# Kernel tuning notes

Measured on AMD Instinct MI355X. Metric: run time of the kernel, lower is better.

Reference implementation:

```python
import jax, jax.numpy as jnp
import numpy as np

B, S, D, V = 64, 16, 2048, 128000


def setup_inputs() -> dict:
    key = jax.random.key(0)
    k1, k2, k3, k4, k5 = jax.random.split(key, 5)
    embedding = jax.random.normal(k1, (V, D), dtype=jnp.float32) * 0.02
    hidden_states = jax.random.normal(k2, (B, S, D), dtype=jnp.float32)
    output_positions = jnp.array([S - 1], dtype=jnp.int32)  # sample from last position
    temperatures = jax.random.uniform(k3, (B,), dtype=jnp.float32, minval=0.5, maxval=1.5)
    top_ps = jax.random.uniform(k4, (B,), dtype=jnp.float32, minval=0.7, maxval=1.0)
    top_ks = jax.random.randint(k5, (B,), 1, 64).astype(jnp.int32)
    return {
        "embedding": embedding,
        "hidden_states": hidden_states,
        "output_positions": output_positions,
        "temperatures": temperatures,
        "top_ps": top_ps,
        "top_ks": top_ks,
    }


def reference(embedding, hidden_states, output_positions, temperatures, top_ps, top_ks):
    # select output position: [B, S, D] -> [B, D]
    hs = jnp.take(hidden_states, output_positions, axis=1)[:, 0, :]
    # vocab logits: [B, V]
    logits = jnp.einsum("bd,vd->bv", hs, embedding)
    logits = logits / temperatures[:, None]
    probs = jax.nn.softmax(logits.astype(jnp.float32), axis=-1)
    # descending sort of probs
    order = jnp.argsort(-probs, axis=-1)                       # [B, V]
    probs_sort = jnp.take_along_axis(probs, order, axis=-1)    # [B, V] descending
    cum = jnp.cumsum(probs_sort, axis=-1)
    # top-p: zero everything whose exclusive-prefix mass exceeds top_p
    probs_sort = jnp.where((cum - probs_sort) > top_ps[:, None], 0.0, probs_sort)
    # top-k: keep only first top_k sorted entries
    ranks = jnp.arange(V, dtype=jnp.int32)[None, :]
    probs_sort = jnp.where(ranks >= top_ks[:, None], 0.0, probs_sort)
    # renormalize
    probs_sort = probs_sort / jnp.sum(probs_sort, axis=-1, keepdims=True)
    # scatter back to original vocab order via inverse permutation
    inv = jnp.argsort(order, axis=-1)
    probs_final = jnp.take_along_axis(probs_sort, inv, axis=-1)
    # multinomial sampling (one token per row); zeros -> log 0 = -inf, excluded
    skey = jax.random.key(42)
    next_token_ids = jax.random.categorical(skey, jnp.log(probs_final), axis=-1)
    return next_token_ids
```

## Files before the change

kernel.cpp:

```cpp
#include <hip/hip_runtime.h>
#include <math.h>

#define BATCH 64
#define SEQ 16
#define DIM 2048
#define VOCAB 128000

#define BM 64
#define BN 128
#define BK 32
#define NT (DIM / BK)

typedef __attribute__((ext_vector_type(8))) short bf16x8;
typedef __attribute__((ext_vector_type(4))) float f32x4;

__device__ __forceinline__ unsigned cvt_pk_bf16(float a, float b) {
  unsigned r;
  asm("v_cvt_pk_bf16_f32 %0, %1, %2" : "=v"(r) : "v"(a), "v"(b));
  return r;
}

__device__ __forceinline__ void split8(float4 x0, float4 x1, bf16x8* hi, bf16x8* lo) {
  float f[8] = {x0.x, x0.y, x0.z, x0.w, x1.x, x1.y, x1.z, x1.w};
  union { unsigned u[4]; bf16x8 v; } H, L;
#pragma unroll
  for (int w = 0; w < 4; ++w) {
    float a = f[2 * w], b = f[2 * w + 1];
    unsigned hp = cvt_pk_bf16(a, b);
    float ha = __uint_as_float(hp << 16);
    float hb = __uint_as_float(hp & 0xffff0000u);
    H.u[w] = hp;
    L.u[w] = cvt_pk_bf16(a - ha, b - hb);
  }
  *hi = H.v;
  *lo = L.v;
}

__device__ __forceinline__ void gload_lds16(const float* src, float* lds_dst) {
  __builtin_amdgcn_global_load_lds(
      (const __attribute__((address_space(1))) void*)src,
      (__attribute__((address_space(3))) void*)lds_dst, 16, 0, 0);
}

__global__ __launch_bounds__(256, 3) void logits_kernel(
    const float* __restrict__ emb,
    const float* __restrict__ hs,
    const int* __restrict__ pos,
    const float* __restrict__ temps,
    float* __restrict__ logits) {
  __shared__ float ldsA[BM * BK];
  __shared__ float ldsB[BN * BK];

  const int tid = threadIdx.x;
  const int lane = tid & 63;
  const int wid = tid >> 6;
  const int lrow = lane & 15;
  const int lkb = lane >> 4;
  const int vb = blockIdx.x * BN + wid * 32;
  const int p = pos[0];

  const int r8 = (lane >> 3) & 7;
  const int c8 = lane & 7;
  const int cswz = 4 * (c8 ^ r8);

  const float* aSrc[2];
  float* aDst[2];
#pragma unroll
  for (int q = 0; q < 2; ++q) {
    const int g = wid * 2 + q;
    const int R = g * 8 + r8;
    aSrc[q] = hs + ((size_t)R * SEQ + p) * DIM + cswz;
    aDst[q] = &ldsA[g * 8 * BK];
  }
  const float* bSrc[4];
  float* bDst[4];
#pragma unroll
  for (int q = 0; q < 4; ++q) {
    const int g = wid * 4 + q;
    const int R = g * 8 + r8;
    bSrc[q] = emb + (size_t)(blockIdx.x * BN + R) * DIM + cswz;
    bDst[q] = &ldsB[g * 8 * BK];
  }

  f32x4 acc[4][2];
#pragma unroll
  for (int i = 0; i < 4; ++i)
#pragma unroll
    for (int j = 0; j < 2; ++j) acc[i][j] = (f32x4){0.f, 0.f, 0.f, 0.f};

  const int sfr = 4 * (lrow & 7);
  const int off0 = (lkb * 8) ^ sfr;
  const int off1 = off0 ^ 4;

  for (int t = 0; t < NT; ++t) {
    const int kof = t * BK;
#pragma unroll
    for (int q = 0; q < 2; ++q) gload_lds16(aSrc[q] + kof, aDst[q]);
#pragma unroll
    for (int q = 0; q < 4; ++q) gload_lds16(bSrc[q] + kof, bDst[q]);
    __syncthreads();

    bf16x8 ah[4], al[4], bh[2], bl[2];
#pragma unroll
    for (int i = 0; i < 4; ++i) {
      const float* rb = &ldsA[(16 * i + lrow) * BK];
      split8(*(const float4*)(rb + off0), *(const float4*)(rb + off1),
             &ah[i], &al[i]);
    }
#pragma unroll
    for (int j = 0; j < 2; ++j) {
      const float* rb = &ldsB[(wid * 32 + 16 * j + lrow) * BK];
      split8(*(const float4*)(rb + off0), *(const float4*)(rb + off1),
             &bh[j], &bl[j]);
    }
#pragma unroll
    for (int i = 0; i < 4; ++i)
#pragma unroll
      for (int j = 0; j < 2; ++j) {
        acc[i][j] = __builtin_amdgcn_mfma_f32_16x16x32_bf16(ah[i], bh[j], acc[i][j], 0, 0, 0);
        acc[i][j] = __builtin_amdgcn_mfma_f32_16x16x32_bf16(ah[i], bl[j], acc[i][j], 0, 0, 0);
        acc[i][j] = __builtin_amdgcn_mfma_f32_16x16x32_bf16(al[i], bh[j], acc[i][j], 0, 0, 0);
      }
    __syncthreads();
  }

#pragma unroll
  for (int i = 0; i < 4; ++i)
#pragma unroll
    for (int r = 0; r < 4; ++r) {
      const int b = 16 * i + lkb * 4 + r;
      const float tt = temps[b];
#pragma unroll
      for (int j = 0; j < 2; ++j) {
        const int v = vb + 16 * j + lrow;
        logits[(size_t)b * VOCAB + v] = acc[i][j][r] / tt;
      }
    }
}

__device__ __forceinline__ void threefry2x32(unsigned k0, unsigned k1,
                                             unsigned x0, unsigned x1,
                                             unsigned* o0, unsigned* o1) {
  const unsigned k2 = k0 ^ k1 ^ 0x1BD11BDAu;
  const unsigned ks[3] = {k0, k1, k2};
  const int rotA[4] = {13, 15, 26, 6};
  const int rotB[4] = {17, 29, 16, 24};
  x0 += k0;
  x1 += k1;
#pragma unroll
  for (int i = 0; i < 5; ++i) {
    const int* rr = (i & 1) ? rotB : rotA;
#pragma unroll
    for (int q = 0; q < 4; ++q) {
      x0 += x1;
      x1 = (x1 << rr[q]) | (x1 >> (32 - rr[q]));
      x1 ^= x0;
    }
    x0 += ks[(i + 1) % 3];
    x1 += ks[(i + 2) % 3] + (unsigned)(i + 1);
  }
  *o0 = x0;
  *o1 = x1;
}

__device__ float gumbel_noise(unsigned flat) {
  unsigned o0, o1;
  threefry2x32(0u, 42u, 0u, flat, &o0, &o1);
  unsigned bits = o0 ^ o1;
  unsigned fb = (bits >> 9) | 0x3f800000u;
  float u = __uint_as_float(fb) - 1.0f;
  const float tiny = 1.17549435e-38f;
  u = fmaxf(u, tiny);
  return -logf(-logf(u));
}

#define CAP 4096
#define NL 12
#define NTH 1024
#define NWAVE 16

__device__ __forceinline__ unsigned sortkey(float x) {
  unsigned bits = __float_as_uint(x);
  return (bits & 0x80000000u) ? ~bits : (bits | 0x80000000u);
}
__device__ __forceinline__ float inv_sortkey(unsigned u) {
  unsigned bits = (u & 0x80000000u) ? (u & 0x7fffffffu) : ~u;
  return __uint_as_float(bits);
}

__global__ __launch_bounds__(NTH) void sample_kernel(
    const float* __restrict__ logits,
    const float* __restrict__ top_ps,
    const int* __restrict__ top_ks,
    const float* __restrict__ temps,
    const int* __restrict__ pos,
    int ws_ok,
    int* __restrict__ out) {
  const int b = blockIdx.x;
  const int tid = threadIdx.x;
  const int lane = tid & 63;
  const int wave = tid >> 6;
  const float* row = logits + (size_t)b * VOCAB;
  const float4* row4 = (const float4*)row;
  const int N4 = VOCAB / 4;

  __shared__ float sred[NWAVE];
  __shared__ int scnt_sh[NL];
  __shared__ float smax, sz;
  __shared__ float sdelta;
  __shared__ unsigned scnt;
  __shared__ unsigned ubuf[CAP];
  __shared__ unsigned ibuf[CAP];
  __shared__ unsigned sorted_u[64];
  __shared__ unsigned sorted_i[64];

  const float D[NL] = {0.5f, 0.75f, 1.0f, 1.25f, 1.5f, 1.75f,
                       2.0f, 2.5f, 3.0f, 4.0f, 8.0f, 1e30f};

  float lmax = -__builtin_huge_valf();
  for (int i = tid; i < N4; i += NTH) {
    float4 v = row4[i];
    lmax = fmaxf(fmaxf(lmax, v.x), fmaxf(fmaxf(v.y, v.z), v.w));
  }
#pragma unroll
  for (int s = 32; s > 0; s >>= 1) lmax = fmaxf(lmax, __shfl_xor(lmax, s, 64));
  if (lane == 0) sred[wave] = lmax;
  if (tid < NL) scnt_sh[tid] = 0;
  __syncthreads();
  if (tid == 0) {
    float m = sred[0];
#pragma unroll
    for (int w = 1; w < NWAVE; ++w) m = fmaxf(m, sred[w]);
    smax = m;
  }
  __syncthreads();
  const float maxl = smax;

  float zsum = 0.f;
  int cnt[NL];
#pragma unroll
  for (int r = 0; r < NL; ++r) cnt[r] = 0;
  for (int i = tid; i < N4; i += NTH) {
    float4 v = row4[i];
    float xs[4] = {v.x, v.y, v.z, v.w};
#pragma unroll
    for (int c = 0; c < 4; ++c) {
      float x = xs[c];
      zsum += expf(x - maxl);
      float d = maxl - x;
#pragma unroll
      for (int r = 0; r < NL; ++r) cnt[r] += (d <= D[r]) ? 1 : 0;
    }
  }
#pragma unroll
  for (int s = 32; s > 0; s >>= 1) {
    zsum += __shfl_xor(zsum, s, 64);
#pragma unroll
    for (int r = 0; r < NL; ++r) cnt[r] += __shfl_xor(cnt[r], s, 64);
  }
  if (lane == 0) {
    sred[wave] = zsum;
#pragma unroll
    for (int r = 0; r < NL; ++r) atomicAdd(&scnt_sh[r], cnt[r]);
  }
  __syncthreads();
  if (tid == 0) {
    float z = 0.f;
#pragma unroll
    for (int w = 0; w < NWAVE; ++w) z += sred[w];
    sz = z;
    float dd = 1e30f;
#pragma unroll
    for (int r = NL - 1; r >= 0; --r)
      if (scnt_sh[r] >= 64) dd = D[r];
    sdelta = dd;
    scnt = 0;
  }
  __syncthreads();
  const float Z = sz;
  const float thrv = maxl - sdelta;

  for (int i = tid; i < N4; i += NTH) {
    float4 v = row4[i];
    float xs[4] = {v.x, v.y, v.z, v.w};
#pragma unroll
    for (int c = 0; c < 4; ++c) {
      if (xs[c] >= thrv) {
        unsigned slot = atomicAdd(&scnt, 1u);
        if (slot < CAP) {
          ubuf[slot] = sortkey(xs[c]);
          ibuf[slot] = (unsigned)(i * 4 + c);
        }
      }
    }
  }
  __syncthreads();
  const int n = (int)(scnt < (unsigned)CAP ? scnt : (unsigned)CAP);

  if (tid < 64) { sorted_u[tid] = 0u; sorted_i[tid] = 0u; }
  __syncthreads();
  for (int c = tid; c < n; c += NTH) {
    unsigned u = ubuf[c], idx = ibuf[c];
    int rank = 0;
    for (int j = 0; j < n; ++j) {
      unsigned uj = ubuf[j];
      rank += (uj > u) || (uj == u && ibuf[j] < idx);
    }
    if (rank < 64) { sorted_u[rank] = u; sorted_i[rank] = idx; }
  }
  __syncthreads();

  if (tid == 0) {
    const float topp = top_ps[b];
    const int k = top_ks[b];
    const float tval = temps[b];
    float cum = 0.f;
    float best = -__builtin_huge_valf();
    int bestidx = 0;
    for (int r = 0; r < 64 && r < n; ++r) {
      float x = inv_sortkey(sorted_u[r]);
      float pr = expf(x - maxl) / Z;
      cum += pr;
      bool keep = (r < k) && !((cum - pr) > topp) && (pr > 0.f);
      if (keep) {
        float g = gumbel_noise((unsigned)b * (unsigned)VOCAB + sorted_i[r]);
        float sc = x + g;
        if (sc > best) { best = sc; bestidx = (int)sorted_i[r]; }
      }
    }
    int token = bestidx;

    unsigned kat0, kat1;
    threefry2x32(0u, 0u, 0u, 0u, &kat0, &kat1);
    bool inputs_ok = (pos[0] >= 0 && pos[0] < SEQ) &&
                     (tval > 0.45f && tval < 1.55f) &&
                     (topp > 0.65f && topp <= 1.0f) &&
                     (k >= 1 && k < 64);
    if (!inputs_ok) token = 3333333;
    else if (!ws_ok) token = 7777777;
    else if (kat0 != 0x6b200159u || kat1 != 0x99ba4efeu) token = 5555555;
    else if (scnt > (unsigned)CAP || n < 64) token = 4444444;
    out[b] = token;
  }
}

extern "C" void kernel_launch(void* const* d_in, const int* in_sizes, int n_in,
                              void* d_out, int out_size, void* d_ws, size_t ws_size,
                              hipStream_t stream) {
  const float* emb   = (const float*)d_in[0];
  const float* hs    = (const float*)d_in[1];
  const int*   pos   = (const int*)d_in[2];
  const float* temps = (const float*)d_in[3];
  const float* topps = (const float*)d_in[4];
  const int*   topks = (const int*)d_in[5];
  float* logits = (float*)d_ws;
  int* out = (int*)d_out;

  const size_t need = (size_t)BATCH * VOCAB * sizeof(float);
  const int ws_ok = (ws_size >= need) ? 1 : 0;

  hipLaunchKernelGGL(logits_kernel, dim3(VOCAB / BN), dim3(256), 0, stream,
                     emb, hs, pos, temps, logits);
  hipLaunchKernelGGL(sample_kernel, dim3(BATCH), dim3(NTH), 0, stream,
                     logits, topps, topks, temps, pos, ws_ok, out);
}
```

Baseline: 345.0 us.

## Double-buffer LDS with register prefetch and XCD-aware block remapping in logits GEMM

Replaces the direct global-to-LDS loads and the two-barrier-per-tile loop with a software pipeline. Global tiles are prefetched into registers two stages ahead and written into one of two LDS buffers, so each tile needs only one barrier. Block indices are remapped so consecutive vocabulary tiles are grouped per XCD. Launch bounds drop to 2 blocks per SM to fit the extra registers and doubled LDS, which lowers occupancy and puts the pipeline in charge of hiding memory latency.

```diff
diff --git a/kernel.cpp b/kernel.cpp
--- a/kernel.cpp
+++ b/kernel.cpp
@@ -10,6 +10,9 @@
 #define BN 128
 #define BK 32
 #define NT (DIM / BK)
+#define ASZ (BM * BK)
+#define BSZ (BN * BK)
+#define NXCD 8
 
 typedef __attribute__((ext_vector_type(8))) short bf16x8;
 typedef __attribute__((ext_vector_type(4))) float f32x4;
@@ -36,50 +39,43 @@
   *lo = L.v;
 }
 
-__device__ __forceinline__ void gload_lds16(const float* src, float* lds_dst) {
-  __builtin_amdgcn_global_load_lds(
-      (const __attribute__((address_space(1))) void*)src,
-      (__attribute__((address_space(3))) void*)lds_dst, 16, 0, 0);
-}
-
-__global__ __launch_bounds__(256, 3) void logits_kernel(
+__global__ __launch_bounds__(256, 2) void logits_kernel(
     const float* __restrict__ emb,
     const float* __restrict__ hs,
     const int* __restrict__ pos,
     const float* __restrict__ temps,
     float* __restrict__ logits) {
-  __shared__ float ldsA[BM * BK];
-  __shared__ float ldsB[BN * BK];
+  __shared__ float ldsA[2 * ASZ];
+  __shared__ float ldsB[2 * BSZ];
 
   const int tid = threadIdx.x;
   const int lane = tid & 63;
   const int wid = tid >> 6;
   const int lrow = lane & 15;
   const int lkb = lane >> 4;
-  const int vb = blockIdx.x * BN + wid * 32;
   const int p = pos[0];
+
+  const int blk = (blockIdx.x & 7) * 125 + (blockIdx.x >> 3);
+  const int vb = blk * BN + wid * 32;
 
   const int r8 = (lane >> 3) & 7;
   const int c8 = lane & 7;
-  const int cswz = 4 * (c8 ^ r8);
 
   const float* aSrc[2];
-  float* aDst[2];
+  float* aDstSw[2];
 #pragma unroll
   for (int q = 0; q < 2; ++q) {
     const int g = wid * 2 + q;
-    const int R = g * 8 + r8;
-    aSrc[q] = hs + ((size_t)R * SEQ + p) * DIM + cswz;
-    aDst[q] = &ldsA[g * 8 * BK];
+    aSrc[q] = hs + ((size_t)(g * 8 + r8) * SEQ + p) * DIM + 4 * c8;
+    aDstSw[q] = &ldsA[(g * 8 + r8) * BK + 4 * (c8 ^ r8)];
   }
   const float* bSrc[4];
-  float* bDst[4];
+  float* bDstSw[4];
 #pragma unroll
   for (int q = 0; q < 4; ++q) {
     const int g = wid * 4 + q;
-    const int R = g * 8 + r8;
-    bSrc[q] = emb + (size_t)(blockIdx.x * BN + R) * DIM + cswz;
-    bDst[q] = &ldsB[g * 8 * BK];
+    bSrc[q] = emb + (size_t)(blk * BN + g * 8 + r8) * DIM + 4 * c8;
+    bDstSw[q] = &ldsB[(g * 8 + r8) * BK + 4 * (c8 ^ r8)];
   }
 
   f32x4 acc[4][2];
@@ -92,37 +88,80 @@
   const int off0 = (lkb * 8) ^ sfr;
   const int off1 = off0 ^ 4;
 
-  for (int t = 0; t < NT; ++t) {
-    const int kof = t * BK;
-#pragma unroll
-    for (int q = 0; q < 2; ++q) gload_lds16(aSrc[q] + kof, aDst[q]);
-#pragma unroll
-    for (int q = 0; q < 4; ++q) gload_lds16(bSrc[q] + kof, bDst[q]);
-    __syncthreads();
-
-    bf16x8 ah[4], al[4], bh[2], bl[2];
-#pragma unroll
-    for (int i = 0; i < 4; ++i) {
-      const float* rb = &ldsA[(16 * i + lrow) * BK];
-      split8(*(const float4*)(rb + off0), *(const float4*)(rb + off1),
-             &ah[i], &al[i]);
-    }
-#pragma unroll
-    for (int j = 0; j < 2; ++j) {
-      const float* rb = &ldsB[(wid * 32 + 16 * j + lrow) * BK];
-      split8(*(const float4*)(rb + off0), *(const float4*)(rb + off1),
-             &bh[j], &bl[j]);
-    }
-#pragma unroll
-    for (int i = 0; i < 4; ++i)
-#pragma unroll
-      for (int j = 0; j < 2; ++j) {
-        acc[i][j] = __builtin_amdgcn_mfma_f32_16x16x32_bf16(ah[i], bh[j], acc[i][j], 0, 0, 0);
-        acc[i][j] = __builtin_amdgcn_mfma_f32_16x16x32_bf16(ah[i], bl[j], acc[i][j], 0, 0, 0);
-        acc[i][j] = __builtin_amdgcn_mfma_f32_16x16x32_bf16(al[i], bh[j], acc[i][j], 0, 0, 0);
-      }
-    __syncthreads();
-  }
+  float4 sa0[2], sb0[4], sa1[2], sb1[4];
+
+#define LOADR(SA, SB, T)                                                  \
+  do {                                                                    \
+    const int kof_ = (T) * BK;                                            \
+    _Pragma("unroll")                                                     \
+    for (int q = 0; q < 2; ++q) SA[q] = *(const float4*)(aSrc[q] + kof_); \
+    _Pragma("unroll")                                                     \
+    for (int q = 0; q < 4; ++q) SB[q] = *(const float4*)(bSrc[q] + kof_); \
+  } while (0)
+
+#define WRITES(SA, SB, BUF)                                               \
+  do {                                                                    \
+    const int ao_ = (BUF) * ASZ;                                          \
+    const int bo_ = (BUF) * BSZ;                                          \
+    _Pragma("unroll")                                                     \
+    for (int q = 0; q < 2; ++q) *(float4*)(aDstSw[q] + ao_) = SA[q];      \
+    _Pragma("unroll")                                                     \
+    for (int q = 0; q < 4; ++q) *(float4*)(bDstSw[q] + bo_) = SB[q];      \
+  } while (0)
+
+#define COMPUTE(BUF)                                                      \
+  do {                                                                    \
+    const float* A_ = &ldsA[(BUF) * ASZ];                                 \
+    const float* B_ = &ldsB[(BUF) * BSZ];                                 \
+    float4 ra[4][2], rb[2][2];                                            \
+    _Pragma("unroll")                                                     \
+    for (int i = 0; i < 4; ++i) {                                         \
+      const float* rbase = &A_[(16 * i + lrow) * BK];                     \
+      ra[i][0] = *(const float4*)(rbase + off0);                          \
+      ra[i][1] = *(const float4*)(rbase + off1);                          \
+    }                                                                     \
+    _Pragma("unroll")                                                     \
+    for (int j = 0; j < 2; ++j) {                                         \
+      const float* rbase = &B_[(wid * 32 + 16 * j + lrow) * BK];          \
+      rb[j][0] = *(const float4*)(rbase + off0);                          \
+      rb[j][1] = *(const float4*)(rbase + off1);                          \
+    }                                                                     \
+    bf16x8 ah[4], al[4], bh[2], bl[2];                                    \
+    _Pragma("unroll")                                                     \
+    for (int i = 0; i < 4; ++i) split8(ra[i][0], ra[i][1], &ah[i], &al[i]);\
+    _Pragma("unroll")                                                     \
+    for (int j = 0; j < 2; ++j) split8(rb[j][0], rb[j][1], &bh[j], &bl[j]);\
+    _Pragma("unroll")                                                     \
+    for (int i = 0; i < 4; ++i)                                           \
+      _Pragma("unroll")                                                   \
+      for (int j = 0; j < 2; ++j) {                                       \
+        acc[i][j] = __builtin_amdgcn_mfma_f32_16x16x32_bf16(ah[i], bh[j], acc[i][j], 0, 0, 0); \
+        acc[i][j] = __builtin_amdgcn_mfma_f32_16x16x32_bf16(ah[i], bl[j], acc[i][j], 0, 0, 0); \
+        acc[i][j] = __builtin_amdgcn_mfma_f32_16x16x32_bf16(al[i], bh[j], acc[i][j], 0, 0, 0); \
+      }                                                                   \
+  } while (0)
+
+  LOADR(sa0, sb0, 0);
+  LOADR(sa1, sb1, 1);
+
+  for (int t = 0; t < NT; t += 2) {
+    WRITES(sa0, sb0, 0);
+    if (t + 2 < NT) LOADR(sa0, sb0, t + 2);
+    asm volatile("s_waitcnt lgkmcnt(0)" ::: "memory");
+    __builtin_amdgcn_sched_barrier(0);
+    __builtin_amdgcn_s_barrier();
+    COMPUTE(0);
+
+    WRITES(sa1, sb1, 1);
+    if (t + 3 < NT) LOADR(sa1, sb1, t + 3);
+    asm volatile("s_waitcnt lgkmcnt(0)" ::: "memory");
+    __builtin_amdgcn_sched_barrier(0);
+    __builtin_amdgcn_s_barrier();
+    COMPUTE(1);
+  }
+#undef LOADR
+#undef WRITES
+#undef COMPUTE
 
 #pragma unroll
   for (int i = 0; i < 4; ++i)
```

Result: slower. 719.7 us (+108.6%).
